# Kernel optimization log

Measured on AMD Instinct MI355X. Metric: run time of the kernel, lower is better.

The kernel has to match this reference:

```python
import jax, jax.numpy as jnp
import numpy as np

N_ENT = 100000
N_REL = 16
DIM = 128
N_LAYERS = 2
N_BASES = 4
N_EDGES = 640000
BATCH = 1024
N_NEG = 64
BN_EPS = 1e-5


def setup_inputs() -> dict:
    key = jax.random.key(0)
    ks = jax.random.split(key, 16)
    inp = {
        'head_idx': jax.random.randint(ks[0], (BATCH,), 0, N_ENT),
        'relation_idx': jax.random.randint(ks[1], (BATCH,), 0, N_REL),
        'tail_idx': jax.random.randint(ks[2], (BATCH,), 0, N_ENT),
        'negative_idx': jax.random.randint(ks[3], (BATCH, N_NEG), 0, N_ENT),
        'edge_index': jax.random.randint(ks[4], (2, N_EDGES), 0, N_ENT),
        'edge_type': jax.random.randint(ks[5], (N_EDGES,), 0, N_REL),
        # learned parameters (xavier-ish scaling)
        'entity_table': jax.random.normal(ks[6], (N_ENT, DIM), jnp.float32) * 0.02,
        'relation_table': jax.random.normal(ks[7], (N_REL, DIM), jnp.float32) * 0.02,
        'bases': jax.random.normal(ks[8], (N_LAYERS, N_BASES, DIM, DIM), jnp.float32) * (1.0 / np.sqrt(DIM)),
        'coeffs': jax.random.normal(ks[9], (N_LAYERS, N_REL, N_BASES), jnp.float32) * 0.5,
        'w_sl': jax.random.normal(ks[10], (N_LAYERS, DIM, DIM), jnp.float32) * (1.0 / np.sqrt(DIM)),
        'b_sl': jnp.zeros((N_LAYERS, DIM), jnp.float32),
        'gamma': jnp.ones((N_LAYERS, DIM), jnp.float32),
        'beta': jnp.zeros((N_LAYERS, DIM), jnp.float32),
    }
    return inp


def _encode(entity_table, bases, coeffs, w_sl, b_sl, gamma, beta, edge_index, edge_type):
    src, dst = edge_index[0], edge_index[1]
    n = entity_table.shape[0]
    # degree normalization (same dst for every layer)
    deg = jnp.zeros((n,), entity_table.dtype).at[dst].add(1.0)
    deg = jnp.maximum(deg, 1.0)[:, None]
    x = entity_table
    for l in range(N_LAYERS):
        # basis decomposition: W[r] = sum_b coeff[r,b] * bases[b]
        W = jnp.einsum('rb,bij->rij', coeffs[l], bases[l])  # [R, d, d]
        out = x @ w_sl[l] + b_sl[l]  # self-loop linear
        # transform all nodes under every relation once, then gather per edge
        H = jnp.einsum('nd,rdf->rnf', x, W)  # [R, N, d]
        msg = H[edge_type, src]  # [E, d]
        out = out.at[dst].add(msg)
        out = out / deg
        # BatchNorm1d (training mode: biased batch stats over nodes)
        mu = jnp.mean(out, axis=0)
        var = jnp.var(out, axis=0)
        out = (out - mu) * jax.lax.rsqrt(var + BN_EPS) * gamma[l] + beta[l]
        x = jax.nn.relu(out)
    return x


def reference(head_idx, relation_idx, tail_idx, negative_idx, edge_index, edge_type,
              entity_table, relation_table, bases, coeffs, w_sl, b_sl, gamma, beta):
    ent = _encode(entity_table, bases, coeffs, w_sl, b_sl, gamma, beta, edge_index, edge_type)
    head = ent[head_idx]                      # [B, d]
    rel = relation_table[relation_idx]        # [B, d]
    tail = ent[tail_idx]                      # [B, d]
    neg = ent[negative_idx]                   # [B, K, d]
    d_pos = head + rel - tail
    pos_score = -jnp.sqrt(jnp.sum(d_pos * d_pos, axis=-1))
    d_neg = (head + rel)[:, None, :] - neg
    neg_score = -jnp.sqrt(jnp.sum(d_neg * d_neg, axis=-1))
    return pos_score, neg_score
```

## Files before the change

kernel.cpp:

```cpp
#include <hip/hip_runtime.h>
#include <stdint.h>

#define N_ENTS  100000
#define N_RELS  16
#define DIM     128
#define NB      4
#define TILE_U  10240
#define NEDGE   640000
#define BATCH   1024
#define NNEG    64
#define BN_EPS  1e-5f
#define BCAP    64
#define SENTR   0x01000000u
#define NPB     32
#define NBLK2   3125

#define B_X     0
#define B_CNT   6250
#define B_TW    6348
#define B_CF    6428
#define B_PAR   6429
#define B_GRID  6440

#define P_REL    0
#define P_BSL    2048
#define P_GAMMA  2304
#define P_BETA   2560
#define P_TOTAL  2816

typedef unsigned int uint;
typedef short short8 __attribute__((ext_vector_type(8)));
typedef float f4 __attribute__((ext_vector_type(4)));

__device__ __forceinline__ float bf2f(unsigned short u) {
    return __uint_as_float(((unsigned int)u) << 16);
}
__device__ __forceinline__ float bflo(unsigned int u) { return __uint_as_float(u << 16); }
__device__ __forceinline__ float bfhi(unsigned int u) { return __uint_as_float(u & 0xffff0000u); }
__device__ __forceinline__ unsigned short f2bf(float f) {
    unsigned int x = __float_as_uint(f);
    x += 0x7fffu + ((x >> 16) & 1u);
    return (unsigned short)(x >> 16);
}
__device__ __forceinline__ unsigned int pack2(float a, float b) {
    return (unsigned int)f2bf(a) | ((unsigned int)f2bf(b) << 16);
}

__device__ __forceinline__ int bf16_like(unsigned int h) {
    unsigned int m = h & 0x7FFFu;
    return (m == 0u) || (m >= 0x2D00u && m < 0x4400u);
}
__global__ __launch_bounds__(256) void k_detect(const unsigned int* __restrict__ ent,
                                                int* __restrict__ flag,
                                                float* __restrict__ stats) {
    __shared__ int cnt[256];
    unsigned int u = ent[threadIdx.x];
    cnt[threadIdx.x] = bf16_like(u & 0xFFFFu) & bf16_like(u >> 16);
    stats[threadIdx.x] = 0.f;
    stats[256 + threadIdx.x] = 0.f;
    __syncthreads();
    for (int s = 128; s > 0; s >>= 1) {
        if (threadIdx.x < s) cnt[threadIdx.x] += cnt[threadIdx.x + s];
        __syncthreads();
    }
    if (threadIdx.x == 0) flag[0] = (cnt[0] >= 140) ? 1 : 0;
}

__device__ __forceinline__ unsigned short cvt1(const void* src, int i, int isbf) {
    return isbf ? ((const unsigned short*)src)[i] : f2bf(((const float*)src)[i]);
}
__global__ __launch_bounds__(256) void k_conv(
    const void* __restrict__ src, unsigned short* __restrict__ xrow,
    const void* __restrict__ rtab, const void* __restrict__ bases,
    const void* __restrict__ coeffs, const void* __restrict__ wsl,
    const void* __restrict__ bsl, const void* __restrict__ gamma,
    const void* __restrict__ beta,
    unsigned short* __restrict__ par, unsigned short* __restrict__ WtT,
    float* __restrict__ cf32, int* __restrict__ cnt, const int* __restrict__ flag)
{
    const int b = blockIdx.x;
    const int isbf = flag[0];
    if (b < B_CNT) {
        if (isbf) return;
        const int kc = threadIdx.x >> 4, r = threadIdx.x & 15;
        const int n = b * 16 + r;
        const size_t e0 = (size_t)n * DIM + kc * 8;
        const float4 f0 = *(const float4*)((const float*)src + e0);
        const float4 f1 = *(const float4*)((const float*)src + e0 + 4);
        uint4 w;
        w.x = pack2(f0.x, f0.y); w.y = pack2(f0.z, f0.w);
        w.z = pack2(f1.x, f1.y); w.w = pack2(f1.z, f1.w);
        *(uint4*)(xrow + e0) = w;
        return;
    }
    if (b < B_TW) {
        const int i = (b - B_CNT) * 256 + threadIdx.x;
        if (i < N_ENTS / 4) {
            uint4 z = {0, 0, 0, 0};
            ((uint4*)cnt)[i] = z;
        }
        return;
    }
    if (b < B_CF) {
        const int i = (b - B_TW) * 256 + threadIdx.x;
        const int l = i / 10240;
        const int rem = i - l * 10240;
        const int jt2 = rem / 1280;
        const int rem2 = rem - jt2 * 1280;
        const int kc = rem2 >> 4, r = rem2 & 15;
        const int n = jt2 * 16 + r;
        unsigned short v[8];
#pragma unroll
        for (int e = 0; e < 8; ++e) {
            const int k = kc * 8 + e;
            v[e] = (k < DIM)
                ? cvt1(wsl,   l * DIM * DIM + k * DIM + n, isbf)
                : cvt1(bases, l * NB * DIM * DIM + (k - DIM) * DIM + n, isbf);
        }
        *(uint4*)(WtT + (size_t)l * 81920 + (size_t)jt2 * TILE_U + (size_t)kc * 128 + r * 8) = *(uint4*)v;
        return;
    }
    if (b == B_CF) {
        const int i = threadIdx.x;
        if (i < 2 * 17 * 4) {
            const int l = i / 68, rem = i - l * 68, r = rem >> 2, bb = rem & 3;
            const int idx = l * N_RELS * NB + r * NB + bb;
            cf32[i] = (r < N_RELS)
                ? (isbf ? bf2f(((const unsigned short*)coeffs)[idx])
                        : ((const float*)coeffs)[idx])
                : 0.f;
        }
        return;
    }
    const int i = (b - B_PAR) * 256 + threadIdx.x;
    if (i >= P_TOTAL) return;
    unsigned short v;
    if      (i < P_BSL)    v = cvt1(rtab,  i - P_REL,   isbf);
    else if (i < P_GAMMA)  v = cvt1(bsl,   i - P_BSL,   isbf);
    else if (i < P_BETA)   v = cvt1(gamma, i - P_GAMMA, isbf);
    else                   v = cvt1(beta,  i - P_BETA,  isbf);
    par[i] = v;
}

__global__ __launch_bounds__(256) void k_fillB(const int* __restrict__ src, const int* __restrict__ dst,
                                               const int* __restrict__ et, int* __restrict__ cnt,
                                               uint* __restrict__ bucket) {
    const int e = blockIdx.x * 256 + threadIdx.x;
    const int d = dst[e];
    const int p = atomicAdd(&cnt[d], 1);
    if (p < BCAP) bucket[(size_t)d * BCAP + p] = (uint)src[e] | ((uint)et[e] << 20);
}

__global__ __launch_bounds__(256, 4) void k_fused(
    const uint* __restrict__ bucket, const int* __restrict__ cnt,
    const float* __restrict__ cf, const unsigned short* __restrict__ xin,
    const void* __restrict__ ent, const int* __restrict__ flag, const int lay,
    const float* __restrict__ stp, const unsigned short* __restrict__ gprev,
    const unsigned short* __restrict__ bprev,
    const unsigned short* __restrict__ wtT, const unsigned short* __restrict__ bsl,
    unsigned short* __restrict__ out, float* __restrict__ pstats)
{
    __shared__ unsigned short Ash[NPB * 640];
    __shared__ __align__(16) uint  bkL[NPB][16];
    __shared__ __align__(16) float cfL[17][4];
    __shared__ int cntL[NPB];
    const int tid = threadIdx.x;
    const int wave = tid >> 6, lane = tid & 63;
    const int n0 = blockIdx.x * NPB;
    const float inv_n = 1.0f / (float)N_ENTS;

    const unsigned short* __restrict__ xs =
        (lay == 0 && flag[0]) ? (const unsigned short*)ent : xin;
    const int mybase = n0 + wave * 8;

    {
        const int nd = wave * 8 + (lane >> 3);
        const int p  = lane & 7;
        const uint2 rv = *(const uint2*)(bucket + (size_t)(n0 + nd) * BCAP + p * 2);
        *(uint2*)&bkL[nd][p * 2] = rv;
        if (lane < 17) {
            const float4 c4 = *(const float4*)(cf + lane * 4);
            *(float4*)&cfL[lane][0] = c4;
        }
        if (lane < 8) cntL[wave * 8 + lane] = cnt[mybase + lane];
    }

    float gnA = 1.f, ofA = 0.f, gnB = 1.f, ofB = 0.f;
    if (lay) {
        const int f0 = lane * 2, f1 = f0 + 1;
        const float mu0 = stp[f0] * inv_n, mu1 = stp[f1] * inv_n;
        const float va0 = stp[DIM + f0] * inv_n - mu0 * mu0;
        const float va1 = stp[DIM + f1] * inv_n - mu1 * mu1;
        gnA = bf2f(gprev[f0]) * rsqrtf(va0 + BN_EPS); ofA = bf2f(bprev[f0]) - mu0 * gnA;
        gnB = bf2f(gprev[f1]) * rsqrtf(va1 + BN_EPS); ofB = bf2f(bprev[f1]) - mu1 * gnB;
    }

    {
        const int r = tid >> 3, c = tid & 7;
        const size_t e0 = (size_t)(n0 + r) * DIM + c * 8;
        uint4 v0 = *(const uint4*)(xs + e0);
        uint4 v1 = *(const uint4*)(xs + e0 + 64);
        if (lay) {
            uint vv[8] = {v0.x, v0.y, v0.z, v0.w, v1.x, v1.y, v1.z, v1.w};
#pragma unroll
            for (int p = 0; p < 8; ++p) {
                const int f0 = c * 8 + (p >> 2) * 64 + (p & 3) * 2;
                const float mu0 = stp[f0] * inv_n, mu1 = stp[f0 + 1] * inv_n;
                const float va0 = stp[DIM + f0] * inv_n - mu0 * mu0;
                const float va1 = stp[DIM + f0 + 1] * inv_n - mu1 * mu1;
                const float g0 = bf2f(gprev[f0]) * rsqrtf(va0 + BN_EPS);
                const float g1 = bf2f(gprev[f0 + 1]) * rsqrtf(va1 + BN_EPS);
                const float o0 = bf2f(bprev[f0]) - mu0 * g0;
                const float o1 = bf2f(bprev[f0 + 1]) - mu1 * g1;
                const float w0 = fmaxf(fmaf(bflo(vv[p]), g0, o0), 0.f);
                const float w1 = fmaxf(fmaf(bfhi(vv[p]), g1, o1), 0.f);
                vv[p] = pack2(w0, w1);
            }
            v0.x = vv[0]; v0.y = vv[1]; v0.z = vv[2]; v0.w = vv[3];
            v1.x = vv[4]; v1.y = vv[5]; v1.z = vv[6]; v1.w = vv[7];
        }
        const int byte0 = (r * 1280 + c * 16) ^ ((r & 7) << 4);
        *(uint4*)((char*)Ash + byte0) = v0;
        *(uint4*)((char*)Ash + byte0 + 128) = v1;
    }

    const uint* __restrict__ x32 = (const uint*)xs;
    for (int pr = 0; pr < 4; ++pr) {
        const int la = wave * 8 + pr * 2;
        const int na = mybase + pr * 2;
        int ca = cntL[la];     if (ca > BCAP) ca = BCAP;
        int cb = cntL[la + 1]; if (cb > BCAP) cb = BCAP;
        const int qm = ((ca > cb ? ca : cb) + 7) >> 3;
        float aLo[2][NB] = {{0.f,0.f,0.f,0.f},{0.f,0.f,0.f,0.f}};
        float aHi[2][NB] = {{0.f,0.f,0.f,0.f},{0.f,0.f,0.f,0.f}};
        const uint4* __restrict__ bkg = (const uint4*)(bucket + (size_t)na * BCAP);
        for (int j = 0; j < qm; ++j) {
            uint rec[2][8];
            uint xw[2][8];
            const int b8 = j * 8;
#pragma unroll
            for (int h = 0; h < 2; ++h) {
                const int cn = h ? cb : ca;
                if (b8 < cn) {
                    if (j < 2) {
#pragma unroll
                        for (int s = 0; s < 8; ++s) rec[h][s] = bkL[la + h][b8 + s];
                    } else {
                        const uint4 r0 = bkg[h * 16 + j * 2];
                        const uint4 r1 = bkg[h * 16 + j * 2 + 1];
                        rec[h][0] = r0.x; rec[h][1] = r0.y; rec[h][2] = r0.z; rec[h][3] = r0.w;
                        rec[h][4] = r1.x; rec[h][5] = r1.y; rec[h][6] = r1.z; rec[h][7] = r1.w;
                    }
#pragma unroll
                    for (int s = 0; s < 8; ++s) {
                        uint rr = rec[h][s];
                        if (b8 + s >= cn) rr = SENTR;
                        rec[h][s] = rr;
                        xw[h][s] = x32[(size_t)(rr & 0xFFFFFu) * 64 + lane];
                    }
                }
            }
#pragma unroll
            for (int h = 0; h < 2; ++h) {
                const int cn = h ? cb : ca;
                if (b8 < cn) {
#pragma unroll
                    for (int s = 0; s < 8; ++s) {
                        const int rel = (int)(rec[h][s] >> 20);
                        const float4 cc = *(const float4*)&cfL[rel][0];
                        float xl, xh;
                        if (lay) {
                            xl = fmaxf(fmaf(bflo(xw[h][s]), gnA, ofA), 0.f);
                            xh = fmaxf(fmaf(bfhi(xw[h][s]), gnB, ofB), 0.f);
                        } else {
                            xl = bflo(xw[h][s]);
                            xh = bfhi(xw[h][s]);
                        }
                        aLo[h][0] = fmaf(cc.x, xl, aLo[h][0]);
                        aHi[h][0] = fmaf(cc.x, xh, aHi[h][0]);
                        aLo[h][1] = fmaf(cc.y, xl, aLo[h][1]);
                        aHi[h][1] = fmaf(cc.y, xh, aHi[h][1]);
                        aLo[h][2] = fmaf(cc.z, xl, aLo[h][2]);
                        aHi[h][2] = fmaf(cc.z, xh, aHi[h][2]);
                        aLo[h][3] = fmaf(cc.w, xl, aLo[h][3]);
                        aHi[h][3] = fmaf(cc.w, xh, aHi[h][3]);
                    }
                }
            }
        }
#pragma unroll
        for (int h = 0; h < 2; ++h) {
            const int ra = wave * 8 + pr * 2 + h;
            const int swz = (ra & 7) << 4;
#pragma unroll
            for (int b = 0; b < NB; ++b) {
                const int byte = (ra * 1280 + 256 + b * 256 + lane * 4) ^ swz;
                *(uint*)((char*)Ash + byte) = pack2(aLo[h][b], aHi[h][b]);
            }
        }
    }

    const int quad = lane >> 4, l16 = lane & 15;
    f4 acc[2][2];
#pragma unroll
    for (int i = 0; i < 2; ++i)
#pragma unroll
        for (int j = 0; j < 2; ++j)
#pragma unroll
            for (int r = 0; r < 4; ++r) acc[i][j][r] = 0.f;

    const unsigned short* __restrict__ pB0 = wtT + (size_t)(2 * wave) * TILE_U + quad * 128 + l16 * 8;
    const unsigned short* __restrict__ pB1 = pB0 + TILE_U;
    const char* Ab = (const char*)Ash;
    const int swz = (l16 & 7) << 4;
    const int b0e = (l16 * 1280 + quad * 16) ^ swz;
    const int b0o = (l16 * 1280 + 64 + quad * 16) ^ swz;
    const int b1e = ((l16 + 16) * 1280 + quad * 16) ^ swz;
    const int b1o = ((l16 + 16) * 1280 + 64 + quad * 16) ^ swz;

    short8 xa0, xa1, xb0, xb1, ya0, ya1, yb0, yb1;
#define FLDA(P, s) \
    P##a0 = *(const short8*)(Ab + (((s) & 1) ? b0o : b0e) + ((s) >> 1) * 128); \
    P##a1 = *(const short8*)(Ab + (((s) & 1) ? b1o : b1e) + ((s) >> 1) * 128);
#define FLDB(P, s) \
    P##b0 = *(const short8*)(pB0 + (s) * 512); \
    P##b1 = *(const short8*)(pB1 + (s) * 512);
#define FLD(P, s) FLDA(P, s) FLDB(P, s)
#define FMM(P) \
    acc[0][0] = __builtin_amdgcn_mfma_f32_16x16x32_bf16(P##a0, P##b0, acc[0][0], 0, 0, 0); \
    acc[0][1] = __builtin_amdgcn_mfma_f32_16x16x32_bf16(P##a0, P##b1, acc[0][1], 0, 0, 0); \
    acc[1][0] = __builtin_amdgcn_mfma_f32_16x16x32_bf16(P##a1, P##b0, acc[1][0], 0, 0, 0); \
    acc[1][1] = __builtin_amdgcn_mfma_f32_16x16x32_bf16(P##a1, P##b1, acc[1][1], 0, 0, 0);

    FLDB(x, 0) FLDB(y, 1)
    __syncthreads();
    FLDA(x, 0) FLDA(y, 1)
    FMM(x) FLD(x, 2)
    FMM(y) FLD(y, 3)
    FMM(x) FLD(x, 4)
    FMM(y) FLD(y, 5)
    FMM(x) FLD(x, 6)
    FMM(y) FLD(y, 7)
    FMM(x) FLD(x, 8)
    FMM(y) FLD(y, 9)
    FMM(x) FLD(x, 10)
    FMM(y) FLD(y, 11)
    FMM(x) FLD(x, 12)
    FMM(y) FLD(y, 13)
    FMM(x) FLD(x, 14)
    FMM(y) FLD(y, 15)
    FMM(x) FLD(x, 16)
    FMM(y) FLD(y, 17)
    FMM(x) FLD(x, 18)
    FMM(y) FLD(y, 19)
    FMM(x)
    FMM(y)
#undef FLDA
#undef FLDB
#undef FLD
#undef FMM

    float ssum[2] = {0.f, 0.f}, sssq[2] = {0.f, 0.f};
#pragma unroll
    for (int m = 0; m < 2; ++m) {
#pragma unroll
        for (int r = 0; r < 4; ++r) {
            const int lrow = m * 16 + quad * 4 + r;
            const int row = n0 + lrow;
            const float rdeg = 1.0f / fmaxf((float)cntL[lrow], 1.0f);
#pragma unroll
            for (int n = 0; n < 2; ++n) {
                const int col = (2 * wave + n) * 16 + l16;
                const float o = (acc[m][n][r] + bf2f(bsl[col])) * rdeg;
                out[(size_t)row * DIM + col] = f2bf(o);
                ssum[n] += o;
                sssq[n] += o * o;
            }
        }
    }
#pragma unroll
    for (int n = 0; n < 2; ++n) {
        float s = ssum[n], q2 = sssq[n];
        s += __shfl_xor(s, 16, 64);  s += __shfl_xor(s, 32, 64);
        q2 += __shfl_xor(q2, 16, 64); q2 += __shfl_xor(q2, 32, 64);
        if (quad == 0) {
            const int col = (2 * wave + n) * 16 + l16;
            pstats[(size_t)blockIdx.x * 256 + col] = s;
            pstats[(size_t)blockIdx.x * 256 + 128 + col] = q2;
        }
    }
}

__global__ __launch_bounds__(256) void k_stats(const float* __restrict__ pstats,
                                               float* __restrict__ st) {
    const int o = threadIdx.x;
    const int b0 = blockIdx.x * 25;
    float s = 0.f;
    for (int b = b0; b < b0 + 25; ++b)
        s += pstats[(size_t)b * 256 + o];
    atomicAdd(&st[o], s);
}

__global__ __launch_bounds__(256) void k_score(
    const int* __restrict__ head, const int* __restrict__ rel,
    const int* __restrict__ tail, const int* __restrict__ negi,
    const unsigned short* __restrict__ emb, const unsigned short* __restrict__ rtab,
    const float* __restrict__ st1, const unsigned short* __restrict__ gm1,
    const unsigned short* __restrict__ bt1,
    void* __restrict__ outp, const int* __restrict__ flag)
{
    const int wave = threadIdx.x >> 6, lane = threadIdx.x & 63;
    const int w = blockIdx.x * 4 + wave;
    const float inv_n = 1.0f / (float)N_ENTS;
    const int f0 = lane * 2, f1 = f0 + 1;
    const float mu0 = st1[f0] * inv_n, mu1 = st1[f1] * inv_n;
    const float va0 = st1[DIM + f0] * inv_n - mu0 * mu0;
    const float va1 = st1[DIM + f1] * inv_n - mu1 * mu1;
    const float g0 = bf2f(gm1[f0]) * rsqrtf(va0 + BN_EPS);
    const float g1 = bf2f(gm1[f1]) * rsqrtf(va1 + BN_EPS);
    const float o0 = bf2f(bt1[f0]) - mu0 * g0;
    const float o1 = bf2f(bt1[f1]) - mu1 * g1;

    int i, t;
    if (w < BATCH) { i = w; t = tail[w]; }
    else { const int w2 = w - BATCH; i = w2 >> 6; t = negi[w2]; }
    const uint hv = ((const uint*)emb)[(size_t)head[i] * 64 + lane];
    const uint rv = ((const uint*)rtab)[(size_t)rel[i] * 64 + lane];
    const uint tv = ((const uint*)emb)[(size_t)t * 64 + lane];
    const float h0 = fmaxf(fmaf(bflo(hv), g0, o0), 0.f);
    const float h1 = fmaxf(fmaf(bfhi(hv), g1, o1), 0.f);
    const float t0 = fmaxf(fmaf(bflo(tv), g0, o0), 0.f);
    const float t1 = fmaxf(fmaf(bfhi(tv), g1, o1), 0.f);
    const float d0 = (h0 + bflo(rv)) - t0;
    const float d1 = (h1 + bfhi(rv)) - t1;
    float s = d0 * d0 + d1 * d1;
#pragma unroll
    for (int m = 32; m >= 1; m >>= 1) s += __shfl_xor(s, m, 64);
    if (lane == 0) {
        const float v = -sqrtf(s);
        if (flag[0]) ((unsigned short*)outp)[w] = f2bf(v);
        else         ((float*)outp)[w] = v;
    }
}

extern "C" void kernel_launch(void* const* d_in, const int* in_sizes, int n_in,
                              void* d_out, int out_size, void* d_ws, size_t ws_size,
                              hipStream_t stream)
{
    const int* head = (const int*)d_in[0];
    const int* rel  = (const int*)d_in[1];
    const int* tail = (const int*)d_in[2];
    const int* negi = (const int*)d_in[3];
    const int* eidx = (const int*)d_in[4];
    const int* etyp = (const int*)d_in[5];
    const void* ent_tab = d_in[6];
    const void* rtab_in = d_in[7];
    const void* bases_in = d_in[8];
    const void* coeffs_in = d_in[9];
    const void* wsl_in = d_in[10];
    const void* bsl_in = d_in[11];
    const void* gamma_in = d_in[12];
    const void* beta_in = d_in[13];

    char* ws = (char*)d_ws;
    size_t off = 0;
    auto alloc = [&](size_t bytes) -> char* {
        char* p = ws + off;
        off += (bytes + 511) & ~(size_t)511;
        return p;
    };
    int* flag            = (int*)alloc(4);
    int* cnt             = (int*)alloc((size_t)N_ENTS * 4);
    uint* bucket         = (uint*)alloc((size_t)N_ENTS * BCAP * 4);
    unsigned short* xrow = (unsigned short*)alloc((size_t)N_ENTS * DIM * 2);
    unsigned short* outA = (unsigned short*)alloc((size_t)N_ENTS * DIM * 2);
    unsigned short* outB = (unsigned short*)alloc((size_t)N_ENTS * DIM * 2);
    unsigned short* par  = (unsigned short*)alloc((size_t)P_TOTAL * 2);
    unsigned short* WtT  = (unsigned short*)alloc((size_t)2 * 81920 * 2);
    float* cf32          = (float*)alloc((size_t)2 * 17 * 4 * 4);
    float* pstats        = (float*)alloc((size_t)NBLK2 * 256 * 4);
    float* stats         = (float*)alloc(2 * 2 * DIM * 4);
    (void)ws_size; (void)in_sizes; (void)n_in; (void)out_size;

    const int* esrc = eidx;
    const int* edst = eidx + NEDGE;

    k_detect<<<1, 256, 0, stream>>>((const unsigned int*)ent_tab, flag, stats);

    k_conv<<<B_GRID, 256, 0, stream>>>(
        ent_tab, xrow, rtab_in, bases_in, coeffs_in, wsl_in, bsl_in, gamma_in, beta_in,
        par, WtT, cf32, cnt, flag);

    k_fillB<<<NEDGE / 256, 256, 0, stream>>>(esrc, edst, etyp, cnt, bucket);

    k_fused<<<NBLK2, 256, 0, stream>>>(
        bucket, cnt, cf32, xrow, ent_tab, flag, 0,
        stats, par + P_GAMMA, par + P_BETA,
        WtT, par + P_BSL, outA, pstats);
    k_stats<<<125, 256, 0, stream>>>(pstats, stats);

    k_fused<<<NBLK2, 256, 0, stream>>>(
        bucket, cnt, cf32 + 68, outA, ent_tab, flag, 1,
        stats, par + P_GAMMA, par + P_BETA,
        WtT + 81920, par + P_BSL + DIM, outB, pstats);
    k_stats<<<125, 256, 0, stream>>>(pstats, stats + 2 * DIM);

    k_score<<<(BATCH + BATCH * NNEG) / 4, 256, 0, stream>>>(
        head, rel, tail, negi, outB, par + P_REL,
        stats + 2 * DIM, par + P_GAMMA + DIM, par + P_BETA + DIM,
        d_out, flag);
}
```

Baseline: 341.6 us.

## Software-pipeline neighbor gathers in fused conv and batch negatives per wave in scoring

Measured after the change: 388.4 us. 1.14x slower.

```diff
diff --git a/kernel.cpp b/kernel.cpp
--- a/kernel.cpp
+++ b/kernel.cpp
@@ -225,72 +225,104 @@
     }
 
     const uint* __restrict__ x32 = (const uint*)xs;
-    for (int pr = 0; pr < 4; ++pr) {
+    uint xwP[2][8], xwQ[2][8];
+
+    auto issue = [&](int pr, uint (&XW)[2][8]) {
         const int la = wave * 8 + pr * 2;
-        const int na = mybase + pr * 2;
+#pragma unroll
+        for (int h = 0; h < 2; ++h) {
+            int cn = cntL[la + h]; if (cn > BCAP) cn = BCAP;
+#pragma unroll
+            for (int s = 0; s < 8; ++s) {
+                uint rr = bkL[la + h][s];
+                if (s >= cn) rr = SENTR;
+                XW[h][s] = x32[(size_t)(rr & 0xFFFFFu) * 64 + lane];
+            }
+        }
+    };
+
+    auto consume = [&](int pr, uint (&XW)[2][8]) {
+        const int la = wave * 8 + pr * 2;
+        const int na = n0 + la;
         int ca = cntL[la];     if (ca > BCAP) ca = BCAP;
         int cb = cntL[la + 1]; if (cb > BCAP) cb = BCAP;
-        const int qm = ((ca > cb ? ca : cb) + 7) >> 3;
         float aLo[2][NB] = {{0.f,0.f,0.f,0.f},{0.f,0.f,0.f,0.f}};
         float aHi[2][NB] = {{0.f,0.f,0.f,0.f},{0.f,0.f,0.f,0.f}};
-        const uint4* __restrict__ bkg = (const uint4*)(bucket + (size_t)na * BCAP);
-        for (int j = 0; j < qm; ++j) {
-            uint rec[2][8];
-            uint xw[2][8];
-            const int b8 = j * 8;
-#pragma unroll
-            for (int h = 0; h < 2; ++h) {
-                const int cn = h ? cb : ca;
-                if (b8 < cn) {
-                    if (j < 2) {
-#pragma unroll
-                        for (int s = 0; s < 8; ++s) rec[h][s] = bkL[la + h][b8 + s];
+#pragma unroll
+        for (int h = 0; h < 2; ++h) {
+            const int cn = h ? cb : ca;
+#pragma unroll
+            for (int s = 0; s < 8; ++s) {
+                const int rel = (s >= cn) ? 16 : (int)(bkL[la + h][s] >> 20);
+                const float4 cc = *(const float4*)&cfL[rel][0];
+                float xl, xh;
+                if (lay) {
+                    xl = fmaxf(fmaf(bflo(XW[h][s]), gnA, ofA), 0.f);
+                    xh = fmaxf(fmaf(bfhi(XW[h][s]), gnB, ofB), 0.f);
+                } else {
+                    xl = bflo(XW[h][s]);
+                    xh = bfhi(XW[h][s]);
+                }
+                aLo[h][0] = fmaf(cc.x, xl, aLo[h][0]);
+                aHi[h][0] = fmaf(cc.x, xh, aHi[h][0]);
+                aLo[h][1] = fmaf(cc.y, xl, aLo[h][1]);
+                aHi[h][1] = fmaf(cc.y, xh, aHi[h][1]);
+                aLo[h][2] = fmaf(cc.z, xl, aLo[h][2]);
+                aHi[h][2] = fmaf(cc.z, xh, aHi[h][2]);
+                aLo[h][3] = fmaf(cc.w, xl, aLo[h][3]);
+                aHi[h][3] = fmaf(cc.w, xh, aHi[h][3]);
+            }
+        }
+#pragma unroll
+        for (int h = 0; h < 2; ++h) {
+            const int cn = h ? cb : ca;
+            const int q = (cn + 7) >> 3;
+            const uint4* __restrict__ bkg = (const uint4*)(bucket + (size_t)(na + h) * BCAP);
+            for (int j = 1; j < q; ++j) {
+                const int b8 = j * 8;
+                uint rec[8], xw[8];
+                if (j < 2) {
+#pragma unroll
+                    for (int s = 0; s < 8; ++s) rec[s] = bkL[la + h][b8 + s];
+                } else {
+                    const uint4 r0 = bkg[j * 2];
+                    const uint4 r1 = bkg[j * 2 + 1];
+                    rec[0] = r0.x; rec[1] = r0.y; rec[2] = r0.z; rec[3] = r0.w;
+                    rec[4] = r1.x; rec[5] = r1.y; rec[6] = r1.z; rec[7] = r1.w;
+                }
+#pragma unroll
+                for (int s = 0; s < 8; ++s) {
+                    uint rr = rec[s];
+                    if (b8 + s >= cn) rr = SENTR;
+                    rec[s] = rr;
+                    xw[s] = x32[(size_t)(rr & 0xFFFFFu) * 64 + lane];
+                }
+#pragma unroll
+                for (int s = 0; s < 8; ++s) {
+                    const int rel = (int)(rec[s] >> 20);
+                    const float4 cc = *(const float4*)&cfL[rel][0];
+                    float xl, xh;
+                    if (lay) {
+                        xl = fmaxf(fmaf(bflo(xw[s]), gnA, ofA), 0.f);
+                        xh = fmaxf(fmaf(bfhi(xw[s]), gnB, ofB), 0.f);
                     } else {
-                        const uint4 r0 = bkg[h * 16 + j * 2];
-                        const uint4 r1 = bkg[h * 16 + j * 2 + 1];
-                        rec[h][0] = r0.x; rec[h][1] = r0.y; rec[h][2] = r0.z; rec[h][3] = r0.w;
-                        rec[h][4] = r1.x; rec[h][5] = r1.y; rec[h][6] = r1.z; rec[h][7] = r1.w;
+                        xl = bflo(xw[s]);
+                        xh = bfhi(xw[s]);
                     }
-#pragma unroll
-                    for (int s = 0; s < 8; ++s) {
-                        uint rr = rec[h][s];
-                        if (b8 + s >= cn) rr = SENTR;
-                        rec[h][s] = rr;
-                        xw[h][s] = x32[(size_t)(rr & 0xFFFFFu) * 64 + lane];
-                    }
+                    aLo[h][0] = fmaf(cc.x, xl, aLo[h][0]);
+                    aHi[h][0] = fmaf(cc.x, xh, aHi[h][0]);
+                    aLo[h][1] = fmaf(cc.y, xl, aLo[h][1]);
+                    aHi[h][1] = fmaf(cc.y, xh, aHi[h][1]);
+                    aLo[h][2] = fmaf(cc.z, xl, aLo[h][2]);
+                    aHi[h][2] = fmaf(cc.z, xh, aHi[h][2]);
+                    aLo[h][3] = fmaf(cc.w, xl, aLo[h][3]);
+                    aHi[h][3] = fmaf(cc.w, xh, aHi[h][3]);
                 }
             }
-#pragma unroll
-            for (int h = 0; h < 2; ++h) {
-                const int cn = h ? cb : ca;
-                if (b8 < cn) {
-#pragma unroll
-                    for (int s = 0; s < 8; ++s) {
-                        const int rel = (int)(rec[h][s] >> 20);
-                        const float4 cc = *(const float4*)&cfL[rel][0];
-                        float xl, xh;
-                        if (lay) {
-                            xl = fmaxf(fmaf(bflo(xw[h][s]), gnA, ofA), 0.f);
-                            xh = fmaxf(fmaf(bfhi(xw[h][s]), gnB, ofB), 0.f);
-                        } else {
-                            xl = bflo(xw[h][s]);
-                            xh = bfhi(xw[h][s]);
-                        }
-                        aLo[h][0] = fmaf(cc.x, xl, aLo[h][0]);
-                        aHi[h][0] = fmaf(cc.x, xh, aHi[h][0]);
-                        aLo[h][1] = fmaf(cc.y, xl, aLo[h][1]);
-                        aHi[h][1] = fmaf(cc.y, xh, aHi[h][1]);
-                        aLo[h][2] = fmaf(cc.z, xl, aLo[h][2]);
-                        aHi[h][2] = fmaf(cc.z, xh, aHi[h][2]);
-                        aLo[h][3] = fmaf(cc.w, xl, aLo[h][3]);
-                        aHi[h][3] = fmaf(cc.w, xh, aHi[h][3]);
-                    }
-                }
-            }
         }
 #pragma unroll
         for (int h = 0; h < 2; ++h) {
-            const int ra = wave * 8 + pr * 2 + h;
+            const int ra = la + h;
             const int swz = (ra & 7) << 4;
 #pragma unroll
             for (int b = 0; b < NB; ++b) {
@@ -298,7 +330,13 @@
                 *(uint*)((char*)Ash + byte) = pack2(aLo[h][b], aHi[h][b]);
             }
         }
-    }
+    };
+
+    issue(0, xwP);
+    issue(1, xwQ); consume(0, xwP);
+    issue(2, xwP); consume(1, xwQ);
+    issue(3, xwQ); consume(2, xwP);
+    consume(3, xwQ);
 
     const int quad = lane >> 4, l16 = lane & 15;
     f4 acc[2][2];
@@ -410,7 +448,7 @@
     void* __restrict__ outp, const int* __restrict__ flag)
 {
     const int wave = threadIdx.x >> 6, lane = threadIdx.x & 63;
-    const int w = blockIdx.x * 4 + wave;
+    const int i = blockIdx.x * 4 + wave;
     const float inv_n = 1.0f / (float)N_ENTS;
     const int f0 = lane * 2, f1 = f0 + 1;
     const float mu0 = st1[f0] * inv_n, mu1 = st1[f1] * inv_n;
@@ -420,26 +458,49 @@
     const float g1 = bf2f(gm1[f1]) * rsqrtf(va1 + BN_EPS);
     const float o0 = bf2f(bt1[f0]) - mu0 * g0;
     const float o1 = bf2f(bt1[f1]) - mu1 * g1;
-
-    int i, t;
-    if (w < BATCH) { i = w; t = tail[w]; }
-    else { const int w2 = w - BATCH; i = w2 >> 6; t = negi[w2]; }
-    const uint hv = ((const uint*)emb)[(size_t)head[i] * 64 + lane];
+    const int isbf = flag[0];
+
+    const uint* __restrict__ x32 = (const uint*)emb;
+    const uint hv = x32[(size_t)head[i] * 64 + lane];
     const uint rv = ((const uint*)rtab)[(size_t)rel[i] * 64 + lane];
-    const uint tv = ((const uint*)emb)[(size_t)t * 64 + lane];
-    const float h0 = fmaxf(fmaf(bflo(hv), g0, o0), 0.f);
-    const float h1 = fmaxf(fmaf(bfhi(hv), g1, o1), 0.f);
-    const float t0 = fmaxf(fmaf(bflo(tv), g0, o0), 0.f);
-    const float t1 = fmaxf(fmaf(bfhi(tv), g1, o1), 0.f);
-    const float d0 = (h0 + bflo(rv)) - t0;
-    const float d1 = (h1 + bfhi(rv)) - t1;
-    float s = d0 * d0 + d1 * d1;
-#pragma unroll
-    for (int m = 32; m >= 1; m >>= 1) s += __shfl_xor(s, m, 64);
-    if (lane == 0) {
-        const float v = -sqrtf(s);
-        if (flag[0]) ((unsigned short*)outp)[w] = f2bf(v);
-        else         ((float*)outp)[w] = v;
+    const float hr0 = fmaxf(fmaf(bflo(hv), g0, o0), 0.f) + bflo(rv);
+    const float hr1 = fmaxf(fmaf(bfhi(hv), g1, o1), 0.f) + bfhi(rv);
+
+    const int tIdx = negi[i * 64 + lane];
+    const uint tvPos = x32[(size_t)tail[i] * 64 + lane];
+
+    auto score1 = [&](uint tvv, int oidx) {
+        const float t0 = fmaxf(fmaf(bflo(tvv), g0, o0), 0.f);
+        const float t1 = fmaxf(fmaf(bfhi(tvv), g1, o1), 0.f);
+        const float d0 = hr0 - t0, d1 = hr1 - t1;
+        float s = d0 * d0 + d1 * d1;
+#pragma unroll
+        for (int m = 32; m >= 1; m >>= 1) s += __shfl_xor(s, m, 64);
+        if (lane == 0) {
+            const float v = -sqrtf(s);
+            if (isbf) ((unsigned short*)outp)[oidx] = f2bf(v);
+            else      ((float*)outp)[oidx] = v;
+        }
+    };
+
+    score1(tvPos, i);
+
+    uint a[8], b[8];
+#pragma unroll
+    for (int k = 0; k < 8; ++k)
+        a[k] = x32[(size_t)__shfl(tIdx, k, 64) * 64 + lane];
+#pragma unroll
+    for (int g = 0; g < 8; ++g) {
+        if (g < 7) {
+#pragma unroll
+            for (int k = 0; k < 8; ++k) {
+                const uint v = x32[(size_t)__shfl(tIdx, (g + 1) * 8 + k, 64) * 64 + lane];
+                if (g & 1) a[k] = v; else b[k] = v;
+            }
+        }
+#pragma unroll
+        for (int k = 0; k < 8; ++k)
+            score1((g & 1) ? b[k] : a[k], BATCH + i * 64 + g * 8 + k);
     }
 }
 
@@ -505,7 +566,7 @@
         WtT + 81920, par + P_BSL + DIM, outB, pstats);
     k_stats<<<125, 256, 0, stream>>>(pstats, stats + 2 * DIM);
 
-    k_score<<<(BATCH + BATCH * NNEG) / 4, 256, 0, stream>>>(
+    k_score<<<BATCH / 4, 256, 0, stream>>>(
         head, rel, tail, negi, outB, par + P_REL,
         stats + 2 * DIM, par + P_GAMMA + DIM, par + P_BETA + DIM,
         d_out, flag);
```
